# Kernel optimization log

Measured on AMD Instinct MI355X. Metric: run time of the kernel, lower is better.

## Reference

```python
import jax, jax.numpy as jnp
import numpy as np

N_EMBD = 1024
N_HEAD = 16


def setup_inputs() -> dict:
    key = jax.random.key(0)
    ks = jax.random.split(key, 5)
    s = 0.02
    x = jax.random.normal(ks[0], (4, 2048, N_EMBD), dtype=jnp.float32)
    W_attn = jax.random.normal(ks[1], (N_EMBD, 3 * N_EMBD), dtype=jnp.float32) * s
    b_attn = jnp.zeros((3 * N_EMBD,), dtype=jnp.float32)
    W_proj = jax.random.normal(ks[2], (N_EMBD, N_EMBD), dtype=jnp.float32) * s
    b_proj = jnp.zeros((N_EMBD,), dtype=jnp.float32)
    return {"x": x, "W_attn": W_attn, "b_attn": b_attn, "W_proj": W_proj, "b_proj": b_proj}


def reference(x, W_attn, b_attn, W_proj, b_proj):
    B, T, C = x.shape
    H = N_HEAD
    D = C // H
    qkv = x @ W_attn + b_attn  # [B,T,3C]
    q, k, v = jnp.split(qkv, 3, axis=-1)
    # [B,H,T,D]
    q = q.reshape(B, T, H, D).transpose(0, 2, 1, 3)
    k = k.reshape(B, T, H, D).transpose(0, 2, 1, 3)
    v = v.reshape(B, T, H, D).transpose(0, 2, 1, 3)
    att = jnp.einsum('bhqd,bhkd->bhqk', q, k) * (1.0 / np.sqrt(D))
    causal = jnp.tril(jnp.ones((T, T), dtype=bool))
    att = jnp.where(causal[None, None], att, -jnp.inf)
    att = jax.nn.softmax(att, axis=-1)
    y = jnp.einsum('bhqk,bhkd->bhqd', att, v)
    y = y.transpose(0, 2, 1, 3).reshape(B, T, C)
    return y @ W_proj + b_proj
```

## Files before the change

### kernel.cpp

```cpp
#include <hip/hip_runtime.h>
#include <hip/hip_bf16.h>

#define B_ 4
#define T_ 2048
#define C_ 1024
#define H_ 16
#define D_ 64
#define N3_ 3072
#define M_ (B_*T_)

typedef __bf16 bf16x8 __attribute__((ext_vector_type(8)));
typedef float f32x4 __attribute__((ext_vector_type(4)));
typedef float f32x16 __attribute__((ext_vector_type(16)));

__device__ __forceinline__ unsigned short f2bf(float f){
  __bf16 h = (__bf16)f;
  return __builtin_bit_cast(unsigned short, h);
}
__device__ __forceinline__ unsigned int pk2(float a, float b){
  return (unsigned int)f2bf(a) | ((unsigned int)f2bf(b)<<16);
}
__device__ __forceinline__ void gload_lds16(const unsigned short* g, unsigned short* l){
  __builtin_amdgcn_global_load_lds(
      (const __attribute__((address_space(1))) void*)g,
      (__attribute__((address_space(3))) void*)l, 16, 0, 0);
}

__device__ __forceinline__ void tr_tile(
    const float* __restrict__ src, unsigned short* __restrict__ dst,
    int K, int N, int bx, int by, float tile[32][33])
{
  const int tx = threadIdx.x & 31, ty = threadIdx.x >> 5;
  const int nt = bx * 32, kt = by * 32;
  #pragma unroll
  for (int i=0;i<32;i+=8) tile[ty+i][tx] = src[(size_t)(kt+ty+i)*N + nt+tx];
  __syncthreads();
  #pragma unroll
  for (int i=0;i<32;i+=8) dst[(size_t)(nt+ty+i)*K + kt+tx] = f2bf(tile[tx][ty+i]);
}

#define XCVT_BLKS (M_*C_/2048)
#define TRA_BLKS  ((N3_/32)*(C_/32))
#define TRP_BLKS  ((C_/32)*(C_/32))

__global__ __launch_bounds__(256) void prep(
    const float* __restrict__ X,  unsigned short* __restrict__ Xb,
    const float* __restrict__ Wa, unsigned short* __restrict__ Wat,
    const float* __restrict__ Wp, unsigned short* __restrict__ Wpt)
{
  __shared__ float tile[32][33];
  const int bid = (int)blockIdx.x;
  if (bid < XCVT_BLKS){
    const size_t i = ((size_t)bid*256 + threadIdx.x)*8;
    float4 f0 = *(const float4*)(X+i);
    float4 f1 = *(const float4*)(X+i+4);
    uint4 w = make_uint4(pk2(f0.x,f0.y), pk2(f0.z,f0.w), pk2(f1.x,f1.y), pk2(f1.z,f1.w));
    *(uint4*)(Xb+i) = w;
  } else if (bid < XCVT_BLKS + TRA_BLKS){
    const int t = bid - XCVT_BLKS;
    tr_tile(Wa, Wat, C_, N3_, t % (N3_/32), t / (N3_/32), tile);
  } else {
    const int t = bid - (XCVT_BLKS + TRA_BLKS);
    tr_tile(Wp, Wpt, C_, C_, t % (C_/32), t / (C_/32), tile);
  }
}

__global__ __launch_bounds__(256) void qkv_gemm(
    const unsigned short* __restrict__ Xb, const unsigned short* __restrict__ Wt,
    const float* __restrict__ bias,
    unsigned short* __restrict__ Qb, unsigned short* __restrict__ Kb,
    unsigned short* __restrict__ Vt)
{
  __shared__ __align__(16) unsigned short As[128][32];
  __shared__ __align__(16) unsigned short Bs[128][32];
  const int tid = threadIdx.x;
  const int nbx = N3_/128;
  const int cpx = (nbx*(M_/128))/8;
  const int id0 = (int)blockIdx.x;
  const int swz = (id0 & 7)*cpx + (id0 >> 3);
  const int m0 = (swz / nbx)*128, n0 = (swz % nbx)*128;
  const int wv = tid>>6, lane = tid&63, lm = lane&15, lq = lane>>4;
  const int wr = wv>>1, wc = wv&1;
  f32x4 acc[4][4] = {};
  const int schunk = (lane&3) ^ ((lane>>3)&3);
  const unsigned short* gA = Xb + (size_t)(m0 + wv*32 + (lane>>2))*C_ + schunk*8;
  const unsigned short* gB = Wt + (size_t)(n0 + wv*32 + (lane>>2))*C_ + schunk*8;
  unsigned short* lA0 = &As[wv*32][0];
  unsigned short* lA1 = &As[wv*32+16][0];
  unsigned short* lB0 = &Bs[wv*32][0];
  unsigned short* lB1 = &Bs[wv*32+16][0];
  const int rkey = (lm>>1)&3;
  for (int k0=0;k0<C_;k0+=32){
    __syncthreads();
    gload_lds16(gA + k0,            lA0);
    gload_lds16(gA + 16*C_ + k0,    lA1);
    gload_lds16(gB + k0,            lB0);
    gload_lds16(gB + 16*C_ + k0,    lB1);
    __syncthreads();
    bf16x8 a[4], b[4];
    #pragma unroll
    for (int mt=0;mt<4;mt++) a[mt] = *(const bf16x8*)&As[wr*64+mt*16+lm][(lq^rkey)*8];
    #pragma unroll
    for (int nt=0;nt<4;nt++) b[nt] = *(const bf16x8*)&Bs[wc*64+nt*16+lm][(lq^rkey)*8];
    #pragma unroll
    for (int mt=0;mt<4;mt++)
      #pragma unroll
      for (int nt=0;nt<4;nt++)
        acc[mt][nt] = __builtin_amdgcn_mfma_f32_16x16x32_bf16(a[mt], b[nt], acc[mt][nt], 0,0,0);
  }
  const int sel = n0>>10;
  const float qsc = (sel==0) ? 0.18033688f : 1.0f;
  #pragma unroll
  for (int mt=0;mt<4;mt++){
    const int grow = m0 + wr*64 + mt*16 + lq*4;
    const int bb = grow>>11, tt0 = grow&2047;
    #pragma unroll
    for (int nt=0;nt<4;nt++){
      const int gcol = n0 + wc*64 + nt*16 + lm;
      const int hh = (gcol>>6)&15, dd = gcol&63;
      const float bv = bias[gcol];
      if (sel==2){
        ushort4 pv;
        pv.x = f2bf(acc[mt][nt][0] + bv);
        pv.y = f2bf(acc[mt][nt][1] + bv);
        pv.z = f2bf(acc[mt][nt][2] + bv);
        pv.w = f2bf(acc[mt][nt][3] + bv);
        *(ushort4*)&Vt[ ((size_t)(bb*H_+hh)*D_ + dd)*T_ + tt0 ] = pv;
      } else {
        unsigned short* dst = (sel==0) ? Qb : Kb;
        #pragma unroll
        for (int r=0;r<4;r++)
          dst[ ((size_t)(bb*H_+hh)*T_ + tt0 + r)*D_ + dd ] = f2bf((acc[mt][nt][r] + bv)*qsc);
      }
    }
  }
}

#define PV_CHUNK(SV, KG, C16) do{                                              \
  unsigned int X0_, X1_, Y0_, Y1_;                                             \
  asm("v_cvt_pk_bf16_f32 %0, %1, %2" : "=v"(X0_)                               \
      : "v"((float)(SV)[(C16)*8+0]), "v"((float)(SV)[(C16)*8+1]));             \
  asm("v_cvt_pk_bf16_f32 %0, %1, %2" : "=v"(X1_)                               \
      : "v"((float)(SV)[(C16)*8+2]), "v"((float)(SV)[(C16)*8+3]));             \
  asm("v_cvt_pk_bf16_f32 %0, %1, %2" : "=v"(Y0_)                               \
      : "v"((float)(SV)[(C16)*8+4]), "v"((float)(SV)[(C16)*8+5]));             \
  asm("v_cvt_pk_bf16_f32 %0, %1, %2" : "=v"(Y1_)                               \
      : "v"((float)(SV)[(C16)*8+6]), "v"((float)(SV)[(C16)*8+7]));             \
  asm volatile("v_permlane32_swap_b32 %0, %1" : "+v"(X0_), "+v"(Y0_));         \
  asm volatile("v_permlane32_swap_b32 %0, %1" : "+v"(X1_), "+v"(Y1_));         \
  uint4 pw_ = make_uint4(X0_, X1_, Y0_, Y1_);                                  \
  bf16x8 pf_ = __builtin_bit_cast(bf16x8, pw_);                                \
  const int ch_ = (((KG)*4 + (C16)*2 + hi) ^ l7)*8;                            \
  bf16x8 v0_ = *(const bf16x8*)&Vs[cb][l31][ch_];                              \
  bf16x8 v1_ = *(const bf16x8*)&Vs[cb][32+l31][ch_];                           \
  o0 = __builtin_amdgcn_mfma_f32_32x32x16_bf16(v0_, pf_, o0, 0,0,0);           \
  o1 = __builtin_amdgcn_mfma_f32_32x32x16_bf16(v1_, pf_, o1, 0,0,0);           \
}while(0)

__global__ __launch_bounds__(256, 3) void flash_attn(
    const unsigned short* __restrict__ Qb, const unsigned short* __restrict__ Kb,
    const unsigned short* __restrict__ Vt, unsigned short* __restrict__ Yb)
{
  __shared__ __align__(16) unsigned short Ks[2][64][64];
  __shared__ __align__(16) unsigned short Vs[2][64][64];
  const int tid = threadIdx.x;
  const int wv = tid>>6, lane = tid&63;
  const int l31 = lane & 31, hi = lane >> 5, l7 = lane & 7;
  const int id = (int)blockIdx.x;
  const int bh = id & 63;
  const int qblk = 15 - (id >> 6);
  const int qb = qblk*128;
  const int q0 = qb + wv*32;
  const unsigned short* Qh = Qb + (size_t)bh*T_*D_;
  const unsigned short* Kh = Kb + (size_t)bh*T_*D_;
  const unsigned short* Vh = Vt + (size_t)bh*D_*T_;
  bf16x8 aq[4];
  #pragma unroll
  for (int kc=0;kc<4;kc++)
    aq[kc] = *(const bf16x8*)&Qh[(size_t)(q0+l31)*D_ + kc*16 + hi*8];
  f32x16 o0 = {}, o1 = {};
  float l_r = 0.f;
  const int srl = lane>>3;
  const int sc  = (lane&7) ^ srl;
  const unsigned short* kg = Kh + (size_t)(wv*16 + srl)*D_ + sc*8;
  const unsigned short* vg = Vh + (size_t)(wv*16 + srl)*T_ + sc*8;
  {
    unsigned short* lk = &Ks[0][wv*16][0];
    unsigned short* lv = &Vs[0][wv*16][0];
    gload_lds16(kg,        lk);
    gload_lds16(kg + 8*D_, lk + 8*64);
    gload_lds16(vg,        lv);
    gload_lds16(vg + 8*T_, lv + 8*64);
  }
  const int JT = 2*qblk + 2;
  const int jmax = 2*qblk + (wv>>1);
  for (int j=0;j<JT;j++){
    const int cb = j&1;
    __syncthreads();
    if (j < JT-1){
      unsigned short* lk = &Ks[cb^1][wv*16][0];
      unsigned short* lv = &Vs[cb^1][wv*16][0];
      gload_lds16(kg + (size_t)((j+1)*64  )*D_, lk);
      gload_lds16(kg + (size_t)((j+1)*64+8)*D_, lk + 8*64);
      gload_lds16(vg + (j+1)*64,                lv);
      gload_lds16(vg + 8*T_ + (j+1)*64,         lv + 8*64);
    }
    if (j <= jmax){
      f32x16 s0 = {}, s1 = {};
      __builtin_amdgcn_s_setprio(1);
      #pragma unroll
      for (int kc=0;kc<4;kc++){
        const int ch = ((kc*2+hi) ^ l7)*8;
        bf16x8 k0 = *(const bf16x8*)&Ks[cb][l31][ch];
        bf16x8 k1 = *(const bf16x8*)&Ks[cb][32+l31][ch];
        s0 = __builtin_amdgcn_mfma_f32_32x32x16_bf16(k0, aq[kc], s0, 0,0,0);
        s1 = __builtin_amdgcn_mfma_f32_32x32x16_bf16(k1, aq[kc], s1, 0,0,0);
      }
      __builtin_amdgcn_s_setprio(0);
      if (j == jmax){
        const int qrel = ((wv&1)<<5) + l31;
        #pragma unroll
        for (int r=0;r<16;r++){
          const int koff = (r&3) + 8*(r>>2) + 4*hi;
          s0[r] = (koff      <= qrel) ? exp2f(s0[r]) : 0.f;
          s1[r] = (32 + koff <= qrel) ? exp2f(s1[r]) : 0.f;
        }
      } else {
        #pragma unroll
        for (int r=0;r<16;r++){ s0[r] = exp2f(s0[r]); s1[r] = exp2f(s1[r]); }
      }
      #pragma unroll
      for (int r=0;r<16;r++) l_r += s0[r] + s1[r];
      __builtin_amdgcn_s_setprio(1);
      PV_CHUNK(s0, 0, 0); PV_CHUNK(s0, 0, 1);
      PV_CHUNK(s1, 1, 0); PV_CHUNK(s1, 1, 1);
      __builtin_amdgcn_s_setprio(0);
    }
  }
  float rs = l_r + __shfl_xor(l_r, 32);
  const float linv = 1.0f / rs;
  const int bb = bh>>4, hh = bh&15;
  const int q = q0 + l31;
  unsigned short* yrow = Yb + (size_t)(bb*T_ + q)*C_ + hh*64;
  #pragma unroll
  for (int g=0; g<4; g++){
    ushort4 y;
    y.x = f2bf(o0[4*g+0]*linv); y.y = f2bf(o0[4*g+1]*linv);
    y.z = f2bf(o0[4*g+2]*linv); y.w = f2bf(o0[4*g+3]*linv);
    *(ushort4*)&yrow[g*8 + hi*4] = y;
    ushort4 z;
    z.x = f2bf(o1[4*g+0]*linv); z.y = f2bf(o1[4*g+1]*linv);
    z.z = f2bf(o1[4*g+2]*linv); z.w = f2bf(o1[4*g+3]*linv);
    *(ushort4*)&yrow[32 + g*8 + hi*4] = z;
  }
}

__global__ __launch_bounds__(256) void proj_gemm(
    const unsigned short* __restrict__ Yb, const unsigned short* __restrict__ Wt,
    const float* __restrict__ bias, float* __restrict__ Out)
{
  __shared__ __align__(16) unsigned short As[128][32];
  __shared__ __align__(16) unsigned short Bs[128][32];
  const int tid = threadIdx.x;
  const int nbx = C_/128;
  const int cpx = (nbx*(M_/128))/8;
  const int id0 = (int)blockIdx.x;
  const int swz = (id0 & 7)*cpx + (id0 >> 3);
  const int m0 = (swz / nbx)*128, n0 = (swz % nbx)*128;
  const int wv = tid>>6, lane = tid&63, lm = lane&15, lq = lane>>4;
  const int wr = wv>>1, wc = wv&1;
  f32x4 acc[4][4] = {};
  const int schunk = (lane&3) ^ ((lane>>3)&3);
  const unsigned short* gA = Yb + (size_t)(m0 + wv*32 + (lane>>2))*C_ + schunk*8;
  const unsigned short* gB = Wt + (size_t)(n0 + wv*32 + (lane>>2))*C_ + schunk*8;
  unsigned short* lA0 = &As[wv*32][0];
  unsigned short* lA1 = &As[wv*32+16][0];
  unsigned short* lB0 = &Bs[wv*32][0];
  unsigned short* lB1 = &Bs[wv*32+16][0];
  const int rkey = (lm>>1)&3;
  for (int k0=0;k0<C_;k0+=32){
    __syncthreads();
    gload_lds16(gA + k0,            lA0);
    gload_lds16(gA + 16*C_ + k0,    lA1);
    gload_lds16(gB + k0,            lB0);
    gload_lds16(gB + 16*C_ + k0,    lB1);
    __syncthreads();
    bf16x8 a[4], b[4];
    #pragma unroll
    for (int mt=0;mt<4;mt++) a[mt] = *(const bf16x8*)&As[wr*64+mt*16+lm][(lq^rkey)*8];
    #pragma unroll
    for (int nt=0;nt<4;nt++) b[nt] = *(const bf16x8*)&Bs[wc*64+nt*16+lm][(lq^rkey)*8];
    #pragma unroll
    for (int mt=0;mt<4;mt++)
      #pragma unroll
      for (int nt=0;nt<4;nt++)
        acc[mt][nt] = __builtin_amdgcn_mfma_f32_16x16x32_bf16(a[mt], b[nt], acc[mt][nt], 0,0,0);
  }
  #pragma unroll
  for (int mt=0;mt<4;mt++){
    const int grow = m0 + wr*64 + mt*16 + lq*4;
    #pragma unroll
    for (int nt=0;nt<4;nt++){
      const int gcol = n0 + wc*64 + nt*16 + lm;
      const float bv = bias[gcol];
      #pragma unroll
      for (int r=0;r<4;r++)
        Out[(size_t)(grow+r)*C_ + gcol] = acc[mt][nt][r] + bv;
    }
  }
}

extern "C" void kernel_launch(void* const* d_in, const int* in_sizes, int n_in,
                              void* d_out, int out_size, void* d_ws, size_t ws_size,
                              hipStream_t stream)
{
  const float* x      = (const float*)d_in[0];
  const float* W_attn = (const float*)d_in[1];
  const float* b_attn = (const float*)d_in[2];
  const float* W_proj = (const float*)d_in[3];
  const float* b_proj = (const float*)d_in[4];
  float* out = (float*)d_out;

  unsigned short* Wat = (unsigned short*)d_ws;
  unsigned short* Wpt = Wat + (size_t)N3_*C_;
  unsigned short* Xb  = Wpt + (size_t)C_*C_;
  unsigned short* Qb  = Xb  + (size_t)M_*C_;
  unsigned short* Kb  = Qb  + (size_t)M_*C_;
  unsigned short* Vt  = Kb  + (size_t)M_*C_;
  unsigned short* Yb  = Vt  + (size_t)M_*C_;
  (void)ws_size; (void)in_sizes; (void)n_in; (void)out_size;

  prep      <<<dim3(XCVT_BLKS+TRA_BLKS+TRP_BLKS), 256, 0, stream>>>(
                x, Xb, W_attn, Wat, W_proj, Wpt);
  qkv_gemm  <<<dim3((N3_/128)*(M_/128)), 256, 0, stream>>>(Xb, Wat, b_attn, Qb, Kb, Vt);
  flash_attn<<<dim3(1024),               256, 0, stream>>>(Qb, Kb, Vt, Yb);
  proj_gemm <<<dim3((C_/128)*(M_/128)),  256, 0, stream>>>(Yb, Wpt, b_proj, out);
}
```

Before: 241.0 us.

## Double-buffer LDS tiles in QKV and projection GEMMs to prefetch next K-slice

Both GEMM kernels get two LDS buffers for the A and B tiles. While the MFMAs run on the current K-slice, the next slice is loaded from global memory into the other buffer. This cuts one of the two barriers per iteration and lets global-to-LDS loads overlap with compute. It doubles LDS use per block, which may lower occupancy, and it relies on the barrier draining the async LDS loads before the data is read.

After: 261.0 us. 1.08x slower.

```diff
diff --git a/kernel.cpp b/kernel.cpp
--- a/kernel.cpp
+++ b/kernel.cpp
@@ -71,8 +71,8 @@
     unsigned short* __restrict__ Qb, unsigned short* __restrict__ Kb,
     unsigned short* __restrict__ Vt)
 {
-  __shared__ __align__(16) unsigned short As[128][32];
-  __shared__ __align__(16) unsigned short Bs[128][32];
+  __shared__ __align__(16) unsigned short As[2][128][32];
+  __shared__ __align__(16) unsigned short Bs[2][128][32];
   const int tid = threadIdx.x;
   const int nbx = N3_/128;
   const int cpx = (nbx*(M_/128))/8;
@@ -85,23 +85,26 @@
   const int schunk = (lane&3) ^ ((lane>>3)&3);
   const unsigned short* gA = Xb + (size_t)(m0 + wv*32 + (lane>>2))*C_ + schunk*8;
   const unsigned short* gB = Wt + (size_t)(n0 + wv*32 + (lane>>2))*C_ + schunk*8;
-  unsigned short* lA0 = &As[wv*32][0];
-  unsigned short* lA1 = &As[wv*32+16][0];
-  unsigned short* lB0 = &Bs[wv*32][0];
-  unsigned short* lB1 = &Bs[wv*32+16][0];
   const int rkey = (lm>>1)&3;
-  for (int k0=0;k0<C_;k0+=32){
+  gload_lds16(gA,          &As[0][wv*32][0]);
+  gload_lds16(gA + 16*C_,  &As[0][wv*32+16][0]);
+  gload_lds16(gB,          &Bs[0][wv*32][0]);
+  gload_lds16(gB + 16*C_,  &Bs[0][wv*32+16][0]);
+  for (int ks=0; ks<32; ks++){
+    const int cb = ks&1;
     __syncthreads();
-    gload_lds16(gA + k0,            lA0);
-    gload_lds16(gA + 16*C_ + k0,    lA1);
-    gload_lds16(gB + k0,            lB0);
-    gload_lds16(gB + 16*C_ + k0,    lB1);
-    __syncthreads();
+    if (ks < 31){
+      const int k1 = (ks+1)*32;
+      gload_lds16(gA + k1,          &As[cb^1][wv*32][0]);
+      gload_lds16(gA + 16*C_ + k1,  &As[cb^1][wv*32+16][0]);
+      gload_lds16(gB + k1,          &Bs[cb^1][wv*32][0]);
+      gload_lds16(gB + 16*C_ + k1,  &Bs[cb^1][wv*32+16][0]);
+    }
     bf16x8 a[4], b[4];
     #pragma unroll
-    for (int mt=0;mt<4;mt++) a[mt] = *(const bf16x8*)&As[wr*64+mt*16+lm][(lq^rkey)*8];
-    #pragma unroll
-    for (int nt=0;nt<4;nt++) b[nt] = *(const bf16x8*)&Bs[wc*64+nt*16+lm][(lq^rkey)*8];
+    for (int mt=0;mt<4;mt++) a[mt] = *(const bf16x8*)&As[cb][wr*64+mt*16+lm][(lq^rkey)*8];
+    #pragma unroll
+    for (int nt=0;nt<4;nt++) b[nt] = *(const bf16x8*)&Bs[cb][wc*64+nt*16+lm][(lq^rkey)*8];
     #pragma unroll
     for (int mt=0;mt<4;mt++)
       #pragma unroll
@@ -259,8 +262,8 @@
     const unsigned short* __restrict__ Yb, const unsigned short* __restrict__ Wt,
     const float* __restrict__ bias, float* __restrict__ Out)
 {
-  __shared__ __align__(16) unsigned short As[128][32];
-  __shared__ __align__(16) unsigned short Bs[128][32];
+  __shared__ __align__(16) unsigned short As[2][128][32];
+  __shared__ __align__(16) unsigned short Bs[2][128][32];
   const int tid = threadIdx.x;
   const int nbx = C_/128;
   const int cpx = (nbx*(M_/128))/8;
@@ -273,23 +276,26 @@
   const int schunk = (lane&3) ^ ((lane>>3)&3);
   const unsigned short* gA = Yb + (size_t)(m0 + wv*32 + (lane>>2))*C_ + schunk*8;
   const unsigned short* gB = Wt + (size_t)(n0 + wv*32 + (lane>>2))*C_ + schunk*8;
-  unsigned short* lA0 = &As[wv*32][0];
-  unsigned short* lA1 = &As[wv*32+16][0];
-  unsigned short* lB0 = &Bs[wv*32][0];
-  unsigned short* lB1 = &Bs[wv*32+16][0];
   const int rkey = (lm>>1)&3;
-  for (int k0=0;k0<C_;k0+=32){
+  gload_lds16(gA,          &As[0][wv*32][0]);
+  gload_lds16(gA + 16*C_,  &As[0][wv*32+16][0]);
+  gload_lds16(gB,          &Bs[0][wv*32][0]);
+  gload_lds16(gB + 16*C_,  &Bs[0][wv*32+16][0]);
+  for (int ks=0; ks<32; ks++){
+    const int cb = ks&1;
     __syncthreads();
-    gload_lds16(gA + k0,            lA0);
-    gload_lds16(gA + 16*C_ + k0,    lA1);
-    gload_lds16(gB + k0,            lB0);
-    gload_lds16(gB + 16*C_ + k0,    lB1);
-    __syncthreads();
+    if (ks < 31){
+      const int k1 = (ks+1)*32;
+      gload_lds16(gA + k1,          &As[cb^1][wv*32][0]);
+      gload_lds16(gA + 16*C_ + k1,  &As[cb^1][wv*32+16][0]);
+      gload_lds16(gB + k1,          &Bs[cb^1][wv*32][0]);
+      gload_lds16(gB + 16*C_ + k1,  &Bs[cb^1][wv*32+16][0]);
+    }
     bf16x8 a[4], b[4];
     #pragma unroll
-    for (int mt=0;mt<4;mt++) a[mt] = *(const bf16x8*)&As[wr*64+mt*16+lm][(lq^rkey)*8];
-    #pragma unroll
-    for (int nt=0;nt<4;nt++) b[nt] = *(const bf16x8*)&Bs[wc*64+nt*16+lm][(lq^rkey)*8];
+    for (int mt=0;mt<4;mt++) a[mt] = *(const bf16x8*)&As[cb][wr*64+mt*16+lm][(lq^rkey)*8];
+    #pragma unroll
+    for (int nt=0;nt<4;nt++) b[nt] = *(const bf16x8*)&Bs[cb][wc*64+nt*16+lm][(lq^rkey)*8];
     #pragma unroll
     for (int mt=0;mt<4;mt++)
       #pragma unroll
```
